# Kernel tuning notes

Measured on AMD Instinct MI355X. Metric: run time of the kernel, lower is better.

## Reference

```python
import jax, jax.numpy as jnp
import numpy as np

N_NODES = 100000
DEG = 16
N_EDGES = N_NODES * DEG
D_IN = 64
D_OUT = 64


def setup_inputs() -> dict:
    key = jax.random.key(0)
    k1, k2, k3 = jax.random.split(key, 3)
    X = jax.random.normal(k1, (N_NODES, D_IN), dtype=jnp.float32)
    stdv = 1.0 / np.sqrt(D_OUT)
    weight = jax.random.uniform(k2, (D_IN, D_OUT), dtype=jnp.float32, minval=-stdv, maxval=stdv)
    # CSR: fixed out-degree DEG per node (regularized for reproducible setup)
    row_pointers = (jnp.arange(N_NODES + 1, dtype=jnp.int64) * DEG)
    column_index = jax.random.randint(k3, (N_EDGES,), 0, N_NODES, dtype=jnp.int32)
    # GCN normalization: degrees[i] = 1/sqrt(d_i)
    counts = (row_pointers[1:] - row_pointers[:-1]).astype(jnp.float32)
    degrees = 1.0 / jnp.sqrt(jnp.maximum(counts, 1.0))
    return {"X": X, "weight": weight, "row_pointers": row_pointers,
            "column_index": column_index, "degrees": degrees}


def reference(X, weight, row_pointers, column_index, degrees):
    # Feature transform first (D_OUT <= D_IN keeps aggregation traffic low)
    xw = X @ weight                                   # [N, D_OUT]
    counts = row_pointers[1:] - row_pointers[:-1]     # [N]
    dst = jnp.repeat(jnp.arange(N_NODES, dtype=jnp.int32), counts,
                     total_repeat_length=N_EDGES)     # [E] destination node per edge
    src = column_index                                # [E] neighbor (source) per edge
    norm = degrees[dst] * degrees[src]                # [E] d_i^{-1/2} d_j^{-1/2}
    msgs = xw[src] * norm[:, None]                    # [E, D_OUT]
    out = jax.ops.segment_sum(msgs, dst, num_segments=N_NODES)  # [N, D_OUT]
    return out
```

## Files before the change

### kernel.cpp

```cpp
#include <hip/hip_runtime.h>
#include <hip/hip_bf16.h>

#define D 64

static __device__ __forceinline__ float bcast_f(float v, int l) {
    return __uint_as_float(__builtin_amdgcn_readlane(__float_as_uint(v), l));
}

__global__ __launch_bounds__(256, 2)
void xw_scale_kernel(const float* __restrict__ X, const float* __restrict__ W,
                     const float* __restrict__ deg, ushort* __restrict__ Y,
                     int n_nodes)
{
    const int lane   = threadIdx.x & 63;
    const int gwave  = (int)((blockIdx.x * blockDim.x + threadIdx.x) >> 6);
    const int nwaves = (int)((gridDim.x * blockDim.x) >> 6);

    float wcol[D];
#pragma unroll
    for (int l = 0; l < D; ++l) wcol[l] = W[l * D + lane];

    for (int node = gwave; node < n_nodes; node += nwaves) {
        const float xr = X[(size_t)node * D + lane];
        const float dn = deg[node];
        float a0 = 0.f, a1 = 0.f, a2 = 0.f, a3 = 0.f;
#pragma unroll
        for (int l = 0; l < D; l += 4) {
            a0 = fmaf(bcast_f(xr, l + 0), wcol[l + 0], a0);
            a1 = fmaf(bcast_f(xr, l + 1), wcol[l + 1], a1);
            a2 = fmaf(bcast_f(xr, l + 2), wcol[l + 2], a2);
            a3 = fmaf(bcast_f(xr, l + 3), wcol[l + 3], a3);
        }
        const float r = ((a0 + a1) + (a2 + a3)) * dn;
        const uint32_t u = __float_as_uint(r);
        Y[(size_t)node * D + lane] = (ushort)((u + 0x7fffu + ((u >> 16) & 1u)) >> 16);
    }
}

__global__ __launch_bounds__(256, 4)
void gather_kernel(const ushort* __restrict__ Y, const int* __restrict__ rp,
                   const int* __restrict__ col, const float* __restrict__ deg,
                   float* __restrict__ out, int n_nodes)
{
    const int lane   = threadIdx.x & 63;
    const int gwave  = (int)((blockIdx.x * blockDim.x + threadIdx.x) >> 6);
    const int nwaves = (int)((gridDim.x * blockDim.x) >> 6);
    const int npairs = (n_nodes + 1) >> 1;

    for (int p = gwave; p < npairs; p += nwaves) {
        const int nA = 2 * p, nB = 2 * p + 1;
        const bool hasB = (nB < n_nodes);
        const int a0 = rp[nA], a1 = rp[nA + 1];
        const int b0 = hasB ? rp[nB] : 0;
        const int b1 = hasB ? rp[nB + 1] : 0;

        if ((a1 - a0) == 16 && (!hasB || (b1 - b0) == 16)) {
            int s_ = 0;
            if (lane < 16)        s_ = col[a0 + lane];
            else if (lane < 32)   s_ = hasB ? col[b0 + (lane & 15)] : 0;

            const int half  = lane >> 5;
            const int feat2 = lane & 31;

            float accx = 0.f, accy = 0.f;
#pragma unroll
            for (int j = 0; j < 16; ++j) {
                const int sa = __builtin_amdgcn_readlane(s_, j);
                const int sb = __builtin_amdgcn_readlane(s_, 16 + j);
                const int s  = half ? sb : sa;
                const uint32_t u =
                    *(const uint32_t*)(Y + (size_t)s * D + feat2 * 2);
                accx += __uint_as_float(u << 16);
                accy += __uint_as_float(u & 0xffff0000u);
            }
            const int nd = half ? nB : nA;
            const float dn = (half && !hasB) ? 0.f : deg[nd];
            if (!half || hasB) {
                float2 v; v.x = accx * dn; v.y = accy * dn;
                *(float2*)(out + (size_t)nd * D + feat2 * 2) = v;
            }
        } else {
            for (int t = 0; t < 2; ++t) {
                const int nd = t ? nB : nA;
                if (nd >= n_nodes) break;
                const int st = rp[nd], en = rp[nd + 1];
                float acc = 0.f;
                for (int e = st; e < en; ++e) {
                    const int s = col[e];
                    const uint32_t w = Y[(size_t)s * D + lane];
                    acc += __uint_as_float(w << 16);
                }
                out[(size_t)nd * D + lane] = acc * deg[nd];
            }
        }
    }
}

__global__ __launch_bounds__(256, 4)
void gcn_fused_kernel(const float* __restrict__ X, const float* __restrict__ W,
                      const int* __restrict__ rp, const int* __restrict__ col,
                      const float* __restrict__ deg, float* __restrict__ out,
                      int n_nodes)
{
    const int lane   = threadIdx.x & 63;
    const int gwave  = (int)((blockIdx.x * blockDim.x + threadIdx.x) >> 6);
    const int nwaves = (int)((gridDim.x * blockDim.x) >> 6);

    for (int node = gwave; node < n_nodes; node += nwaves) {
        const int start = rp[node];
        const int end   = rp[node + 1];
        const float di  = deg[node];
        float h0 = 0.f, h1 = 0.f, h2 = 0.f, h3 = 0.f;

        for (int e0 = start; e0 < end; e0 += 64) {
            const int cnt = min(64, end - e0);
            int   s_  = (lane < cnt) ? col[e0 + lane] : 0;
            float nm_ = (lane < cnt) ? di * deg[s_] : 0.f;
            for (int j = 0; j < cnt; ++j) {
                const int   sj = __builtin_amdgcn_readlane(s_, j);
                const float nj = bcast_f(nm_, j);
                h0 = fmaf(nj, X[(size_t)sj * D + lane], h0);
            }
        }
        const float h = (h0 + h1) + (h2 + h3);

        float c0 = 0.f, c1 = 0.f, c2 = 0.f, c3 = 0.f;
#pragma unroll
        for (int l = 0; l < D; l += 4) {
            c0 = fmaf(bcast_f(h, l + 0), W[(l + 0) * D + lane], c0);
            c1 = fmaf(bcast_f(h, l + 1), W[(l + 1) * D + lane], c1);
            c2 = fmaf(bcast_f(h, l + 2), W[(l + 2) * D + lane], c2);
            c3 = fmaf(bcast_f(h, l + 3), W[(l + 3) * D + lane], c3);
        }
        out[(size_t)node * D + lane] = (c0 + c1) + (c2 + c3);
    }
}

extern "C" void kernel_launch(void* const* d_in, const int* in_sizes, int n_in,
                              void* d_out, int out_size, void* d_ws, size_t ws_size,
                              hipStream_t stream) {
    const float* X   = (const float*)d_in[0];
    const float* W   = (const float*)d_in[1];
    const int*   rp  = (const int*)d_in[2];
    const int*   col = (const int*)d_in[3];
    const float* deg = (const float*)d_in[4];
    float* out = (float*)d_out;

    const int n_nodes = in_sizes[4];
    const size_t y_bytes = (size_t)n_nodes * D * sizeof(ushort);

    if (ws_size >= y_bytes) {
        ushort* Y = (ushort*)d_ws;
        xw_scale_kernel<<<1024, 256, 0, stream>>>(X, W, deg, Y, n_nodes);
        gather_kernel<<<2048, 256, 0, stream>>>(Y, rp, col, deg, out, n_nodes);
    } else {
        gcn_fused_kernel<<<1024, 256, 0, stream>>>(X, W, rp, col, deg, out, n_nodes);
    }
}
```

Baseline: 132.8 us.

## Gather four nodes per wave with vectorized index and bf16x4 loads

The gather kernel now assigns four destination nodes to each wave, using 16 lanes per node. Each lane loads the node's 16 column indices as int4 vectors and reads 4 bf16 features (8 bytes) per neighbour, replacing the readlane broadcast of indices across two nodes. The transform kernel now reads X rows directly through uniform, scalar-friendly loads instead of lane broadcasts, and its occupancy hint is raised to 4. The fast path requires every node in the group to have degree 16 with 16-byte-aligned row offsets; any group that fails this falls back to a per-node loop.

```diff
diff --git a/kernel.cpp b/kernel.cpp
--- a/kernel.cpp
+++ b/kernel.cpp
@@ -1,99 +1,99 @@
 #include <hip/hip_runtime.h>
-#include <hip/hip_bf16.h>
 
 #define D 64
 
-static __device__ __forceinline__ float bcast_f(float v, int l) {
-    return __uint_as_float(__builtin_amdgcn_readlane(__float_as_uint(v), l));
-}
-
-__global__ __launch_bounds__(256, 2)
-void xw_scale_kernel(const float* __restrict__ X, const float* __restrict__ W,
-                     const float* __restrict__ deg, ushort* __restrict__ Y,
-                     int n_nodes)
+__global__ __launch_bounds__(256, 4)
+void gcn_xw_mv(const float* __restrict__ X, const float* __restrict__ W,
+               const float* __restrict__ deg, ushort* __restrict__ Y,
+               int n_nodes)
 {
     const int lane   = threadIdx.x & 63;
-    const int gwave  = (int)((blockIdx.x * blockDim.x + threadIdx.x) >> 6);
+    const int gwave  = __builtin_amdgcn_readfirstlane(
+                          (int)((blockIdx.x * blockDim.x + threadIdx.x) >> 6));
     const int nwaves = (int)((gridDim.x * blockDim.x) >> 6);
 
-    float wcol[D];
+    float w[D];
 #pragma unroll
-    for (int l = 0; l < D; ++l) wcol[l] = W[l * D + lane];
+    for (int l = 0; l < D; ++l) w[l] = W[l * D + lane];
 
     for (int node = gwave; node < n_nodes; node += nwaves) {
-        const float xr = X[(size_t)node * D + lane];
-        const float dn = deg[node];
+        const float* __restrict__ xr = X + (size_t)node * D;
         float a0 = 0.f, a1 = 0.f, a2 = 0.f, a3 = 0.f;
 #pragma unroll
         for (int l = 0; l < D; l += 4) {
-            a0 = fmaf(bcast_f(xr, l + 0), wcol[l + 0], a0);
-            a1 = fmaf(bcast_f(xr, l + 1), wcol[l + 1], a1);
-            a2 = fmaf(bcast_f(xr, l + 2), wcol[l + 2], a2);
-            a3 = fmaf(bcast_f(xr, l + 3), wcol[l + 3], a3);
+            a0 = fmaf(xr[l + 0], w[l + 0], a0);
+            a1 = fmaf(xr[l + 1], w[l + 1], a1);
+            a2 = fmaf(xr[l + 2], w[l + 2], a2);
+            a3 = fmaf(xr[l + 3], w[l + 3], a3);
         }
-        const float r = ((a0 + a1) + (a2 + a3)) * dn;
+        const float r = ((a0 + a1) + (a2 + a3)) * deg[node];
         const uint32_t u = __float_as_uint(r);
         Y[(size_t)node * D + lane] = (ushort)((u + 0x7fffu + ((u >> 16) & 1u)) >> 16);
     }
 }
 
 __global__ __launch_bounds__(256, 4)
-void gather_kernel(const ushort* __restrict__ Y, const int* __restrict__ rp,
-                   const int* __restrict__ col, const float* __restrict__ deg,
-                   float* __restrict__ out, int n_nodes)
+void gcn_gather4(const ushort* __restrict__ Y, const int* __restrict__ rp,
+                 const int* __restrict__ col, const float* __restrict__ deg,
+                 float* __restrict__ out, int n_nodes)
 {
     const int lane   = threadIdx.x & 63;
+    const int s      = lane >> 4;
+    const int f      = lane & 15;
     const int gwave  = (int)((blockIdx.x * blockDim.x + threadIdx.x) >> 6);
     const int nwaves = (int)((gridDim.x * blockDim.x) >> 6);
-    const int npairs = (n_nodes + 1) >> 1;
+    const int ngroups = (n_nodes + 3) >> 2;
 
-    for (int p = gwave; p < npairs; p += nwaves) {
-        const int nA = 2 * p, nB = 2 * p + 1;
-        const bool hasB = (nB < n_nodes);
-        const int a0 = rp[nA], a1 = rp[nA + 1];
-        const int b0 = hasB ? rp[nB] : 0;
-        const int b1 = hasB ? rp[nB + 1] : 0;
+    for (int g = gwave; g < ngroups; g += nwaves) {
+        const int  n     = g * 4 + s;
+        const bool valid = (n < n_nodes);
+        const int  rpn   = valid ? rp[n]     : 0;
+        const int  rpe   = valid ? rp[n + 1] : 0;
+        const int  dcnt  = rpe - rpn;
 
-        if ((a1 - a0) == 16 && (!hasB || (b1 - b0) == 16)) {
-            int s_ = 0;
-            if (lane < 16)        s_ = col[a0 + lane];
-            else if (lane < 32)   s_ = hasB ? col[b0 + (lane & 15)] : 0;
+        const bool ok = !valid || (dcnt == 16 && (rpn & 3) == 0);
+        if (__ballot(ok) == ~0ull) {
+            int idx[16];
+            *(int4*)(idx + 0)  = *(const int4*)(col + rpn + 0);
+            *(int4*)(idx + 4)  = *(const int4*)(col + rpn + 4);
+            *(int4*)(idx + 8)  = *(const int4*)(col + rpn + 8);
+            *(int4*)(idx + 12) = *(const int4*)(col + rpn + 12);
 
-            const int half  = lane >> 5;
-            const int feat2 = lane & 31;
-
-            float accx = 0.f, accy = 0.f;
+            float a0 = 0.f, a1 = 0.f, a2 = 0.f, a3 = 0.f;
 #pragma unroll
             for (int j = 0; j < 16; ++j) {
-                const int sa = __builtin_amdgcn_readlane(s_, j);
-                const int sb = __builtin_amdgcn_readlane(s_, 16 + j);
-                const int s  = half ? sb : sa;
-                const uint32_t u =
-                    *(const uint32_t*)(Y + (size_t)s * D + feat2 * 2);
-                accx += __uint_as_float(u << 16);
-                accy += __uint_as_float(u & 0xffff0000u);
+                const uint2 u = *(const uint2*)(Y + ((size_t)idx[j] << 6) + (f << 2));
+                a0 += __uint_as_float(u.x << 16);
+                a1 += __uint_as_float(u.x & 0xffff0000u);
+                a2 += __uint_as_float(u.y << 16);
+                a3 += __uint_as_float(u.y & 0xffff0000u);
             }
-            const int nd = half ? nB : nA;
-            const float dn = (half && !hasB) ? 0.f : deg[nd];
-            if (!half || hasB) {
-                float2 v; v.x = accx * dn; v.y = accy * dn;
-                *(float2*)(out + (size_t)nd * D + feat2 * 2) = v;
+            if (valid) {
+                const float dn = deg[n];
+                float4 v;
+                v.x = a0 * dn; v.y = a1 * dn; v.z = a2 * dn; v.w = a3 * dn;
+                *(float4*)(out + (size_t)n * D + f * 4) = v;
             }
-        } else {
-            for (int t = 0; t < 2; ++t) {
-                const int nd = t ? nB : nA;
-                if (nd >= n_nodes) break;
-                const int st = rp[nd], en = rp[nd + 1];
-                float acc = 0.f;
-                for (int e = st; e < en; ++e) {
-                    const int s = col[e];
-                    const uint32_t w = Y[(size_t)s * D + lane];
-                    acc += __uint_as_float(w << 16);
-                }
-                out[(size_t)nd * D + lane] = acc * deg[nd];
+        } else if (valid) {
+            float a0 = 0.f, a1 = 0.f, a2 = 0.f, a3 = 0.f;
+            for (int e = rpn; e < rpe; ++e) {
+                const int sj = col[e];
+                const uint2 u = *(const uint2*)(Y + ((size_t)sj << 6) + (f << 2));
+                a0 += __uint_as_float(u.x << 16);
+                a1 += __uint_as_float(u.x & 0xffff0000u);
+                a2 += __uint_as_float(u.y << 16);
+                a3 += __uint_as_float(u.y & 0xffff0000u);
             }
+            const float dn = deg[n];
+            float4 v;
+            v.x = a0 * dn; v.y = a1 * dn; v.z = a2 * dn; v.w = a3 * dn;
+            *(float4*)(out + (size_t)n * D + f * 4) = v;
         }
     }
+}
+
+static __device__ __forceinline__ float bcast_f(float v, int l) {
+    return __uint_as_float(__builtin_amdgcn_readlane(__float_as_uint(v), l));
 }
 
 __global__ __launch_bounds__(256, 4)
@@ -110,7 +110,7 @@
         const int start = rp[node];
         const int end   = rp[node + 1];
         const float di  = deg[node];
-        float h0 = 0.f, h1 = 0.f, h2 = 0.f, h3 = 0.f;
+        float h = 0.f;
 
         for (int e0 = start; e0 < end; e0 += 64) {
             const int cnt = min(64, end - e0);
@@ -119,10 +119,9 @@
             for (int j = 0; j < cnt; ++j) {
                 const int   sj = __builtin_amdgcn_readlane(s_, j);
                 const float nj = bcast_f(nm_, j);
-                h0 = fmaf(nj, X[(size_t)sj * D + lane], h0);
+                h = fmaf(nj, X[(size_t)sj * D + lane], h);
             }
         }
-        const float h = (h0 + h1) + (h2 + h3);
 
         float c0 = 0.f, c1 = 0.f, c2 = 0.f, c3 = 0.f;
 #pragma unroll
@@ -151,8 +150,8 @@
 
     if (ws_size >= y_bytes) {
         ushort* Y = (ushort*)d_ws;
-        xw_scale_kernel<<<1024, 256, 0, stream>>>(X, W, deg, Y, n_nodes);
-        gather_kernel<<<2048, 256, 0, stream>>>(Y, rp, col, deg, out, n_nodes);
+        gcn_xw_mv<<<1024, 256, 0, stream>>>(X, W, deg, Y, n_nodes);
+        gcn_gather4<<<2048, 256, 0, stream>>>(Y, rp, col, deg, out, n_nodes);
     } else {
         gcn_fused_kernel<<<1024, 256, 0, stream>>>(X, W, rp, col, deg, out, n_nodes);
     }
```

After: 178.7 us. 1.35x slower.
